# Optimization experiments

Measured on AMD Instinct MI355X. Metric: run time of the kernel, lower is better.

Reference implementation:

```python
import jax, jax.numpy as jnp
import numpy as np

HEADS = 8
DIM_HEAD = 32
TOP_K = 256
KMEANS_ITERS = 10
EPS_LN = 1e-6
EPS_L2 = 1e-12


def chan_layer_norm(x, gamma, beta):
    # x: (b, c, L); normalize across channel dim (biased variance)
    mean = jnp.mean(x, axis=1, keepdims=True)
    var = jnp.var(x, axis=1, keepdims=True)
    return gamma * (x - mean) / (jnp.sqrt(var) + EPS_LN) + beta


def l2norm_ch(t):
    # F.normalize(t, dim=1): L2-normalize over channel axis of (B, c, L)
    n = jnp.linalg.norm(t, axis=1, keepdims=True)
    return t / jnp.maximum(n, EPS_L2)


def conv1x1(x, w):
    # x: (b, c_in, L), w: (c_out, c_in)  -> (b, c_out, L)
    return jnp.einsum('oc,bcl->bol', w, x)


def _dist2(x, c):
    # squared L2 distances, x: (N, d), c: (k, d) -> (N, k)
    return (jnp.sum(x * x, -1, keepdims=True)
            - 2.0 * x @ c.T
            + jnp.sum(c * c, -1)[None, :])


def kmeans_fit(x, k, iters):
    # Lloyd's algorithm, deterministic init = first k points
    c0 = x[:k]

    def step(c, _):
        assign = jnp.argmin(_dist2(x, c), axis=-1)           # (N,)
        sums = jax.ops.segment_sum(x, assign, num_segments=k)
        cnts = jax.ops.segment_sum(jnp.ones((x.shape[0],), x.dtype), assign,
                                   num_segments=k)
        new_c = jnp.where(cnts[:, None] > 0,
                          sums / jnp.maximum(cnts, 1.0)[:, None], c)
        return new_c, None

    c, _ = jax.lax.scan(step, c0, None, length=iters)
    return c


def select_best_ind(q, k, v, top_k):
    # q: (B, Lq, d), k/v: (B, Lk, d); B = b*heads
    B, Lk, d = k.shape
    q_flat = q.reshape(-1, d)
    centroids = kmeans_fit(q_flat, top_k, KMEANS_ITERS)       # (top_k, d)
    k_flat = k.reshape(-1, d)
    k_cluster = jnp.argmin(_dist2(k_flat, centroids), axis=-1).reshape(B, Lk)
    k_centers = centroids[k_cluster]                          # (B, Lk, d)
    k_dist = jnp.sum(jnp.abs(k_centers - k), axis=-1)         # (B, Lk)
    _, best_k = jax.lax.top_k(k_dist, top_k)                  # largest dists
    idx = best_k[:, :, None]
    k_sel = jnp.take_along_axis(k, idx, axis=1)
    v_sel = jnp.take_along_axis(v, idx, axis=1)
    return k_sel, v_sel


def reference(query_source, context, w_q, w_kv, w_out,
              ln_ctx_gamma, ln_ctx_beta, ln_q_gamma, ln_q_beta,
              ln_out_gamma, ln_out_beta, gamma_scale):
    b, c, L_query = query_source.shape
    ctx = chan_layer_norm(context, ln_ctx_gamma, ln_ctx_beta)
    qs = chan_layer_norm(query_source, ln_q_gamma, ln_q_beta)

    kv = conv1x1(ctx, w_kv)                                   # (b, 2*inner, Lc)
    k, v = jnp.split(kv, 2, axis=1)
    q = conv1x1(qs, w_q)                                      # (b, inner, Lq)

    def fold(t):  # b (h c) L -> (b h) c L
        B, hc, L = t.shape
        return t.reshape(B, HEADS, DIM_HEAD, L).reshape(B * HEADS, DIM_HEAD, L)

    q, k, v = fold(q), fold(k), fold(v)
    q, k = l2norm_ch(q), l2norm_ch(k)
    # b d L -> b L d
    q = jnp.swapaxes(q, 1, 2)
    k = jnp.swapaxes(k, 1, 2)
    v = jnp.swapaxes(v, 1, 2)

    k, v = select_best_ind(q, k, v, TOP_K)

    sim = jnp.einsum('bid,bjd->bij', q, k)                    # (b*h, Lq, top_k)
    attn = jax.nn.softmax(sim, axis=-1)
    out = jnp.einsum('bij,bjd->bid', attn, v)                 # (b*h, Lq, dh)

    out = out.reshape(b, HEADS, L_query, DIM_HEAD)
    out = jnp.transpose(out, (0, 1, 3, 2)).reshape(b, HEADS * DIM_HEAD, L_query)
    out = conv1x1(out, w_out)
    out = chan_layer_norm(out, ln_out_gamma, ln_out_beta)
    return gamma_scale[0] * out + query_source


def setup_inputs() -> dict:
    key = jax.random.key(0)
    ks = jax.random.split(key, 8)
    dim, inner = 256, HEADS * DIM_HEAD
    b, Lq, Lc = 2, 4096, 4096
    inp = {
        'query_source': jax.random.normal(ks[0], (b, dim, Lq), jnp.float32),
        'context': jax.random.normal(ks[1], (b, dim, Lc), jnp.float32),
        'w_q': jax.random.normal(ks[2], (inner, dim), jnp.float32) * 0.05,
        'w_kv': jax.random.normal(ks[3], (2 * inner, dim), jnp.float32) * 0.05,
        'w_out': jax.random.normal(ks[4], (dim, inner), jnp.float32) * 0.05,
        'ln_ctx_gamma': jnp.ones((1, dim, 1), jnp.float32),
        'ln_ctx_beta': jnp.zeros((1, dim, 1), jnp.float32),
        'ln_q_gamma': jnp.ones((1, dim, 1), jnp.float32),
        'ln_q_beta': jnp.zeros((1, dim, 1), jnp.float32),
        'ln_out_gamma': jnp.ones((1, dim, 1), jnp.float32),
        'ln_out_beta': jnp.zeros((1, dim, 1), jnp.float32),
        'gamma_scale': jax.random.normal(ks[5], (1,), jnp.float32),
    }
    return inp
```

## Files before the change

kernel.cpp:

```cpp
#include <hip/hip_runtime.h>
#include <math.h>

#define CDIM 256
#define LSEQ 4096
#define NBH 16
#define NPTS 65536
#define KC 256

__device__ __forceinline__ float fadd(float a, float b){ return __fadd_rn(a,b); }
__device__ __forceinline__ float fmul(float a, float b){ return __fmul_rn(a,b); }
__device__ __forceinline__ float fsub(float a, float b){ return __fsub_rn(a,b); }

__device__ __forceinline__ float sum32_np(const float* e){
    float l[16];
    #pragma unroll
    for (int j = 0; j < 16; j++) l[j] = fadd(e[j], e[j + 16]);
    float t3[8];
    #pragma unroll
    for (int j = 0; j < 8; j++) t3[j] = fadd(l[j], l[j + 8]);
    float t6[4];
    #pragma unroll
    for (int j = 0; j < 4; j++) t6[j] = fadd(t3[j], t3[j + 4]);
    return fadd(fadd(t6[0], t6[2]), fadd(t6[1], t6[3]));
}

__global__ __launch_bounds__(64) void ln2_np(
        const float* __restrict__ x0, const float* __restrict__ g0,
        const float* __restrict__ bt0, float* __restrict__ y0,
        const float* __restrict__ x1, const float* __restrict__ g1,
        const float* __restrict__ bt1, float* __restrict__ y1) {
    int gid = blockIdx.x * 64 + threadIdx.x;
    int which = gid >> 13;
    int r = gid & 8191;
    int b = r >> 12, l = r & 4095;
    const float* x  = which ? x1 : x0;
    const float* g  = which ? g1 : g0;
    const float* bt = which ? bt1 : bt0;
    float* y        = which ? y1 : y0;
    const float* xb = x + (size_t)b * CDIM * LSEQ + l;
    float s = 0.f;
    #pragma unroll 8
    for (int c = 0; c < 256; c++) s = fadd(s, xb[(size_t)c * LSEQ]);
    float mean = __fdiv_rn(s, 256.f);
    float s2 = 0.f;
    #pragma unroll 8
    for (int c = 0; c < 256; c++) {
        float d = fsub(xb[(size_t)c * LSEQ], mean);
        s2 = fadd(s2, fmul(d, d));
    }
    float var = __fdiv_rn(s2, 256.f);
    float den = fadd(__fsqrt_rn(var), 1e-6f);
    float* yb = y + (size_t)b * CDIM * LSEQ + l;
    #pragma unroll 4
    for (int c = 0; c < 256; c++) {
        float d = fsub(xb[(size_t)c * LSEQ], mean);
        yb[(size_t)c * LSEQ] = fadd(__fdiv_rn(fmul(g[c], d), den), bt[c]);
    }
}

__global__ __launch_bounds__(256) void conv_all16(
        const float* __restrict__ Wkv, const float* __restrict__ Xkv,
        float* __restrict__ Ykv,
        const float* __restrict__ Wq, const float* __restrict__ Xq,
        float* __restrict__ Yq) {
    __shared__ float ws[16 * 256];
    int tid = threadIdx.x;
    int l0 = blockIdx.x * 512 + tid * 2;
    bool qpath = blockIdx.y >= 32;
    int yb = qpath ? (blockIdx.y - 32) : blockIdx.y;
    int o0 = yb * 16;
    int b = blockIdx.z;
    const float* W = qpath ? Wq : Wkv;
    const float* X = qpath ? Xq : Xkv;
    {
        const float4* wb4 = (const float4*)(W + (size_t)o0 * CDIM);
        float4* ws4s = (float4*)ws;
        for (int i = tid; i < 16 * 64; i += 256) ws4s[i] = wb4[i];
    }
    __syncthreads();
    const float* xb = X + (size_t)b * CDIM * LSEQ;
    float acc[16][2];
    #pragma unroll
    for (int oo = 0; oo < 16; oo++) { acc[oo][0] = 0.f; acc[oo][1] = 0.f; }
    const float4* ws4 = (const float4*)ws;
    bool sop = qpath || (blockIdx.y < 16);
    if (sop) {
        for (int c = 0; c < 256; c += 4) {
            float2 x0q = *(const float2*)(xb + (size_t)(c + 0) * LSEQ + l0);
            float2 x1q = *(const float2*)(xb + (size_t)(c + 1) * LSEQ + l0);
            float2 x2q = *(const float2*)(xb + (size_t)(c + 2) * LSEQ + l0);
            float2 x3q = *(const float2*)(xb + (size_t)(c + 3) * LSEQ + l0);
            #pragma unroll
            for (int oo = 0; oo < 16; oo++) {
                float4 w = ws4[(oo * 256 + c) >> 2];
                acc[oo][0] = fadd(acc[oo][0], fmul(w.x, x0q.x));
                acc[oo][0] = fadd(acc[oo][0], fmul(w.y, x1q.x));
                acc[oo][0] = fadd(acc[oo][0], fmul(w.z, x2q.x));
                acc[oo][0] = fadd(acc[oo][0], fmul(w.w, x3q.x));
                acc[oo][1] = fadd(acc[oo][1], fmul(w.x, x0q.y));
                acc[oo][1] = fadd(acc[oo][1], fmul(w.y, x1q.y));
                acc[oo][1] = fadd(acc[oo][1], fmul(w.z, x2q.y));
                acc[oo][1] = fadd(acc[oo][1], fmul(w.w, x3q.y));
            }
        }
    } else {
        for (int c = 0; c < 256; c += 4) {
            float2 x0q = *(const float2*)(xb + (size_t)(c + 0) * LSEQ + l0);
            float2 x1q = *(const float2*)(xb + (size_t)(c + 1) * LSEQ + l0);
            float2 x2q = *(const float2*)(xb + (size_t)(c + 2) * LSEQ + l0);
            float2 x3q = *(const float2*)(xb + (size_t)(c + 3) * LSEQ + l0);
            #pragma unroll
            for (int oo = 0; oo < 16; oo++) {
                float4 w = ws4[(oo * 256 + c) >> 2];
                acc[oo][0] = __builtin_fmaf(w.x, x0q.x, acc[oo][0]);
                acc[oo][0] = __builtin_fmaf(w.y, x1q.x, acc[oo][0]);
                acc[oo][0] = __builtin_fmaf(w.z, x2q.x, acc[oo][0]);
                acc[oo][0] = __builtin_fmaf(w.w, x3q.x, acc[oo][0]);
                acc[oo][1] = __builtin_fmaf(w.x, x0q.y, acc[oo][1]);
                acc[oo][1] = __builtin_fmaf(w.y, x1q.y, acc[oo][1]);
                acc[oo][1] = __builtin_fmaf(w.z, x2q.y, acc[oo][1]);
                acc[oo][1] = __builtin_fmaf(w.w, x3q.y, acc[oo][1]);
            }
        }
    }
    float* Y = qpath ? Yq : Ykv;
    int rows = qpath ? 256 : 512;
    #pragma unroll
    for (int oo = 0; oo < 16; oo++)
        *(float2*)(Y + ((size_t)b * rows + o0 + oo) * LSEQ + l0) =
            make_float2(acc[oo][0], acc[oo][1]);
}

template<bool EXACT>
__global__ __launch_bounds__(256) void conv_q8(const float* __restrict__ W,
        const float* __restrict__ X, float* __restrict__ Y) {
    __shared__ float ws[8 * 256];
    int tid = threadIdx.x;
    int l0 = blockIdx.x * 1024 + tid * 4;
    int o0 = blockIdx.y * 8;
    int b = blockIdx.z;
    {
        const float4* wb4 = (const float4*)(W + (size_t)o0 * CDIM);
        float4* ws4s = (float4*)ws;
        for (int i = tid; i < 8 * 64; i += 256) ws4s[i] = wb4[i];
    }
    __syncthreads();
    const float* xb = X + (size_t)b * CDIM * LSEQ;
    float acc[8][4];
    #pragma unroll
    for (int oo = 0; oo < 8; oo++)
        #pragma unroll
        for (int i = 0; i < 4; i++) acc[oo][i] = 0.f;
    const float4* ws4 = (const float4*)ws;
    for (int c = 0; c < 256; c += 4) {
        float4 x0q = *(const float4*)(xb + (size_t)(c + 0) * LSEQ + l0);
        float4 x1q = *(const float4*)(xb + (size_t)(c + 1) * LSEQ + l0);
        float4 x2q = *(const float4*)(xb + (size_t)(c + 2) * LSEQ + l0);
        float4 x3q = *(const float4*)(xb + (size_t)(c + 3) * LSEQ + l0);
        #pragma unroll
        for (int oo = 0; oo < 8; oo++) {
            float4 w = ws4[(oo * 256 + c) >> 2];
            if (EXACT) {
                acc[oo][0] = fadd(acc[oo][0], fmul(w.x, x0q.x));
                acc[oo][0] = fadd(acc[oo][0], fmul(w.y, x1q.x));
                acc[oo][0] = fadd(acc[oo][0], fmul(w.z, x2q.x));
                acc[oo][0] = fadd(acc[oo][0], fmul(w.w, x3q.x));
                acc[oo][1] = fadd(acc[oo][1], fmul(w.x, x0q.y));
                acc[oo][1] = fadd(acc[oo][1], fmul(w.y, x1q.y));
                acc[oo][1] = fadd(acc[oo][1], fmul(w.z, x2q.y));
                acc[oo][1] = fadd(acc[oo][1], fmul(w.w, x3q.y));
                acc[oo][2] = fadd(acc[oo][2], fmul(w.x, x0q.z));
                acc[oo][2] = fadd(acc[oo][2], fmul(w.y, x1q.z));
                acc[oo][2] = fadd(acc[oo][2], fmul(w.z, x2q.z));
                acc[oo][2] = fadd(acc[oo][2], fmul(w.w, x3q.z));
                acc[oo][3] = fadd(acc[oo][3], fmul(w.x, x0q.w));
                acc[oo][3] = fadd(acc[oo][3], fmul(w.y, x1q.w));
                acc[oo][3] = fadd(acc[oo][3], fmul(w.z, x2q.w));
                acc[oo][3] = fadd(acc[oo][3], fmul(w.w, x3q.w));
            } else {
                acc[oo][0] = __builtin_fmaf(w.x, x0q.x, acc[oo][0]);
                acc[oo][0] = __builtin_fmaf(w.y, x1q.x, acc[oo][0]);
                acc[oo][0] = __builtin_fmaf(w.z, x2q.x, acc[oo][0]);
                acc[oo][0] = __builtin_fmaf(w.w, x3q.x, acc[oo][0]);
                acc[oo][1] = __builtin_fmaf(w.x, x0q.y, acc[oo][1]);
                acc[oo][1] = __builtin_fmaf(w.y, x1q.y, acc[oo][1]);
                acc[oo][1] = __builtin_fmaf(w.z, x2q.y, acc[oo][1]);
                acc[oo][1] = __builtin_fmaf(w.w, x3q.y, acc[oo][1]);
                acc[oo][2] = __builtin_fmaf(w.x, x0q.z, acc[oo][2]);
                acc[oo][2] = __builtin_fmaf(w.y, x1q.z, acc[oo][2]);
                acc[oo][2] = __builtin_fmaf(w.z, x2q.z, acc[oo][2]);
                acc[oo][2] = __builtin_fmaf(w.w, x3q.z, acc[oo][2]);
                acc[oo][3] = __builtin_fmaf(w.x, x0q.w, acc[oo][3]);
                acc[oo][3] = __builtin_fmaf(w.y, x1q.w, acc[oo][3]);
                acc[oo][3] = __builtin_fmaf(w.z, x2q.w, acc[oo][3]);
                acc[oo][3] = __builtin_fmaf(w.w, x3q.w, acc[oo][3]);
            }
        }
    }
    #pragma unroll
    for (int oo = 0; oo < 8; oo++)
        *(float4*)(Y + ((size_t)b * 256 + o0 + oo) * LSEQ + l0) =
            make_float4(acc[oo][0], acc[oo][1], acc[oo][2], acc[oo][3]);
}

__device__ __forceinline__ void fold_body(const float* __restrict__ src,
        int srcRows, int row0, int donorm, float* __restrict__ dst,
        float* __restrict__ xxout, float* __restrict__ centout,
        float* __restrict__ ccout, int p) {
    int bh = p >> 12, l = p & 4095;
    int b = bh >> 3, h = bh & 7;
    const float* sp = src + ((size_t)b * srcRows + row0 + h * 32) * LSEQ + l;
    float x[32];
    #pragma unroll
    for (int t = 0; t < 32; t++) x[t] = sp[(size_t)t * LSEQ];
    float4* dp4 = (float4*)(dst + (size_t)p * 32);
    if (donorm) {
        float ss = 0.f;
        #pragma unroll
        for (int t = 0; t < 32; t++) ss = fadd(ss, fmul(x[t], x[t]));
        float n = __fsqrt_rn(ss);
        float den = fmaxf(n, 1e-12f);
        #pragma unroll
        for (int t = 0; t < 32; t++) x[t] = __fdiv_rn(x[t], den);
    }
    #pragma unroll
    for (int t = 0; t < 8; t++)
        dp4[t] = make_float4(x[4*t], x[4*t+1], x[4*t+2], x[4*t+3]);
    if (xxout) {
        float e[32];
        #pragma unroll
        for (int t = 0; t < 32; t++) e[t] = fmul(x[t], x[t]);
        float xv = sum32_np(e);
        xxout[p] = xv;
        if (centout && p < KC) {
            float4* cp4 = (float4*)(centout + (size_t)p * 32);
            #pragma unroll
            for (int t = 0; t < 8; t++)
                cp4[t] = make_float4(x[4*t], x[4*t+1], x[4*t+2], x[4*t+3]);
            ccout[p] = xv;
        }
    }
}

__global__ __launch_bounds__(256) void fold3_np(const float* __restrict__ kvbuf,
        const float* __restrict__ qbuf, float* __restrict__ k_t,
        float* __restrict__ v_t, float* __restrict__ q_t,
        float* __restrict__ xx, float* __restrict__ cent, float* __restrict__ cc) {
    int blk = blockIdx.x, tid = threadIdx.x;
    if (blk < 256) {
        fold_body(kvbuf, 512, 0, 1, k_t, nullptr, nullptr, nullptr, blk * 256 + tid);
    } else if (blk < 512) {
        fold_body(kvbuf, 512, 256, 0, v_t, nullptr, nullptr, nullptr, (blk - 256) * 256 + tid);
    } else {
        fold_body(qbuf, 256, 0, 1, q_t, xx, cent, cc, (blk - 512) * 256 + tid);
    }
}

__global__ __launch_bounds__(256) void assign4p(const float* __restrict__ pts,
        const float* __restrict__ xx, const float* __restrict__ cent,
        const float* __restrict__ cc, int* __restrict__ asn, int* __restrict__ hist) {
    __shared__ float sc[8192];
    __shared__ float scc[256];
    __shared__ int bins[256];
    int tid = threadIdx.x, c = blockIdx.x;
    {
        const float4* c4 = (const float4*)cent;
        float4* s4 = (float4*)sc;
        for (int i = tid; i < 2048; i += 256) s4[i] = c4[i];
    }
    scc[tid] = cc[tid];
    bins[tid] = 0;
    __syncthreads();
    int pg = tid >> 2, quarter = tid & 3;
    int pb = c * 256 + pg * 4;
    float x[4][32];
    float xp[4];
    #pragma unroll
    for (int i = 0; i < 4; i++) {
        const float4* pp = (const float4*)(pts + (size_t)(pb + i) * 32);
        #pragma unroll
        for (int t = 0; t < 8; t++) {
            float4 f = pp[t];
            x[i][4*t] = f.x; x[i][4*t+1] = f.y; x[i][4*t+2] = f.z; x[i][4*t+3] = f.w;
        }
        xp[i] = xx[pb + i];
    }
    float bd[4] = {3.4e38f, 3.4e38f, 3.4e38f, 3.4e38f};
    int bj[4] = {0, 0, 0, 0};
    int jbase = quarter * 64;
    for (int jj = 0; jj < 64; jj++) {
        int j = jbase + jj;
        const float4* cj = (const float4*)(sc + j * 32);
        float w[32];
        #pragma unroll
        for (int t = 0; t < 8; t++) {
            float4 f = cj[t];
            w[4*t] = f.x; w[4*t+1] = f.y; w[4*t+2] = f.z; w[4*t+3] = f.w;
        }
        float sj = scc[j];
        #pragma unroll
        for (int i = 0; i < 4; i++) {
            float g = 0.f;
            #pragma unroll
            for (int t = 0; t < 32; t++) g = __builtin_fmaf(x[i][t], w[t], g);
            float d = fadd(fsub(xp[i], fmul(2.f, g)), sj);
            if (d < bd[i]) { bd[i] = d; bj[i] = j; }
        }
    }
    #pragma unroll
    for (int i = 0; i < 4; i++) {
        float ob; int oj;
        ob = __shfl_xor(bd[i], 1); oj = __shfl_xor(bj[i], 1);
        if (ob < bd[i]) { bd[i] = ob; bj[i] = oj; }
        ob = __shfl_xor(bd[i], 2); oj = __shfl_xor(bj[i], 2);
        if (ob < bd[i]) { bd[i] = ob; bj[i] = oj; }
    }
    if (quarter == 0) {
        #pragma unroll
        for (int i = 0; i < 4; i++) {
            asn[pb + i] = bj[i];
            atomicAdd(&bins[bj[i]], 1);
        }
    }
    __syncthreads();
    hist[c * 256 + tid] = bins[tid];
}

__global__ __launch_bounds__(256) void scan_chunks(const int* __restrict__ hist,
        int* __restrict__ chunkbase, int* __restrict__ totals) {
    __shared__ int a[256];
    int j = blockIdx.x, c = threadIdx.x;
    a[c] = hist[(size_t)c * 256 + j];
    __syncthreads();
    for (int d = 1; d < 256; d <<= 1) {
        int v = a[c];
        int u = (c >= d) ? a[c - d] : 0;
        __syncthreads();
        a[c] = v + u;
        __syncthreads();
    }
    chunkbase[(size_t)c * 256 + j] = (c == 0) ? 0 : a[c - 1];
    if (c == 255) totals[j] = a[255];
}

__global__ __launch_bounds__(256) void scatter_v5(const int* __restrict__ asn,
        const int* __restrict__ chunkbase, const int* __restrict__ totals,
        int* __restrict__ perm) {
    __shared__ int cb[256];
    __shared__ int al[256];
    int c = blockIdx.x, tid = threadIdx.x;
    cb[tid] = totals[tid];
    al[tid] = asn[c * 256 + tid];
    __syncthreads();
    for (int d = 1; d < 256; d <<= 1) {
        int v = cb[tid];
        int u = (tid >= d) ? cb[tid - d] : 0;
        __syncthreads();
        cb[tid] = v + u;
        __syncthreads();
    }
    int my = al[tid];
    int base = (my == 0) ? 0 : cb[my - 1];
    int r = 0;
    for (int i = 0; i < tid; i++) r += (al[i] == my) ? 1 : 0;
    perm[base + chunkbase[(size_t)c * 256 + my] + r] = c * 256 + tid;
}

#define STILE 128
__global__ __launch_bounds__(256) void sumk_v4(const float* __restrict__ pts,
        const int* __restrict__ perm, const int* __restrict__ totals,
        float* __restrict__ cent, float* __restrict__ cc) {
    __shared__ int cb[256];
    __shared__ float buf[2][STILE][32];
    int j = blockIdx.x, tid = threadIdx.x;
    cb[tid] = totals[tid];
    __syncthreads();
    for (int d = 1; d < 256; d <<= 1) {
        int v = cb[tid];
        int u = (tid >= d) ? cb[tid - d] : 0;
        __syncthreads();
        cb[tid] = v + u;
        __syncthreads();
    }
    int base = (j == 0) ? 0 : cb[j - 1];
    int n = totals[j];
    int t = tid & 31, r0 = tid >> 5;
    for (int r = r0; r < STILE; r += 8) {
        if (r < n) buf[0][r][t] = pts[(size_t)perm[base + r] * 32 + t];
    }
    __syncthreads();
    float s = 0.f;
    int b = 0;
    for (int i0 = 0; i0 < n; i0 += STILE, b ^= 1) {
        int nx = i0 + STILE;
        if (nx < n) {
            for (int r = r0; r < STILE; r += 8) {
                int g = nx + r;
                if (g < n) buf[b ^ 1][r][t] = pts[(size_t)perm[base + g] * 32 + t];
            }
        }
        if (tid < 32) {
            int m = n - i0; if (m > STILE) m = STILE;
            int i = 0;
            for (; i + 4 <= m; i += 4) {
                s = fadd(s, buf[b][i][tid]);
                s = fadd(s, buf[b][i + 1][tid]);
                s = fadd(s, buf[b][i + 2][tid]);
                s = fadd(s, buf[b][i + 3][tid]);
            }
            for (; i < m; i++) s = fadd(s, buf[b][i][tid]);
        }
        __syncthreads();
    }
    if (tid < 32) {
        float v;
        if (n > 0) {
            v = __fdiv_rn(s, (float)n);
            cent[(size_t)j * 32 + tid] = v;
        } else {
            v = cent[(size_t)j * 32 + tid];
        }
        float e = fmul(v, v);
        e = fadd(e, __shfl_xor(e, 16));
        e = fadd(e, __shfl_xor(e, 8));
        e = fadd(e, __shfl_xor(e, 4));
        e = fadd(e, __shfl_xor(e, 2));
        e = fadd(e, __shfl_xor(e, 1));
        if (tid == 0) cc[j] = e;
    }
}

__global__ __launch_bounds__(256) void kdist4p(const float* __restrict__ pts,
        const float* __restrict__ cent, const float* __restrict__ cc,
        float* __restrict__ kd) {
    __shared__ float sc[8192];
    __shared__ float scc[256];
    int tid = threadIdx.x, c = blockIdx.x;
    {
        const float4* c4 = (const float4*)cent;
        float4* s4 = (float4*)sc;
        for (int i = tid; i < 2048; i += 256) s4[i] = c4[i];
    }
    scc[tid] = cc[tid];
    __syncthreads();
    int pg = tid >> 2, quarter = tid & 3;
    int pb = c * 256 + pg * 4;
    float x[4][32];
    float xp[4];
    #pragma unroll
    for (int i = 0; i < 4; i++) {
        const float4* pp = (const float4*)(pts + (size_t)(pb + i) * 32);
        #pragma unroll
        for (int t = 0; t < 8; t++) {
            float4 f = pp[t];
            x[i][4*t] = f.x; x[i][4*t+1] = f.y; x[i][4*t+2] = f.z; x[i][4*t+3] = f.w;
        }
        float e[32];
        #pragma unroll
        for (int t = 0; t < 32; t++) e[t] = fmul(x[i][t], x[i][t]);
        xp[i] = sum32_np(e);
    }
    float bd[4] = {3.4e38f, 3.4e38f, 3.4e38f, 3.4e38f};
    int bj[4] = {0, 0, 0, 0};
    int jbase = quarter * 64;
    for (int jj = 0; jj < 64; jj++) {
        int j = jbase + jj;
        const float4* cj = (const float4*)(sc + j * 32);
        float w[32];
        #pragma unroll
        for (int t = 0; t < 8; t++) {
            float4 f = cj[t];
            w[4*t] = f.x; w[4*t+1] = f.y; w[4*t+2] = f.z; w[4*t+3] = f.w;
        }
        float sj = scc[j];
        #pragma unroll
        for (int i = 0; i < 4; i++) {
            float g = 0.f;
            #pragma unroll
            for (int t = 0; t < 32; t++) g = __builtin_fmaf(x[i][t], w[t], g);
            float d = fadd(fsub(xp[i], fmul(2.f, g)), sj);
            if (d < bd[i]) { bd[i] = d; bj[i] = j; }
        }
    }
    #pragma unroll
    for (int i = 0; i < 4; i++) {
        float ob; int oj;
        ob = __shfl_xor(bd[i], 1); oj = __shfl_xor(bj[i], 1);
        if (ob < bd[i]) { bd[i] = ob; bj[i] = oj; }
        ob = __shfl_xor(bd[i], 2); oj = __shfl_xor(bj[i], 2);
        if (ob < bd[i]) { bd[i] = ob; bj[i] = oj; }
    }
    if (quarter == 0) {
        #pragma unroll
        for (int i = 0; i < 4; i++) {
            const float* cb = &sc[bj[i] * 32];
            float e[32];
            #pragma unroll
            for (int t = 0; t < 32; t++) e[t] = fabsf(fsub(cb[t], x[i][t]));
            kd[pb + i] = sum32_np(e);
        }
    }
}

__global__ __launch_bounds__(256) void topk_v3(const float* __restrict__ kd,
        const float* __restrict__ k_t, const float* __restrict__ v_t,
        float* __restrict__ ksel, float* __restrict__ vsel) {
    __shared__ int wsum[4];
    __shared__ int sc1[256];
    __shared__ int out_src[256];
    int bh = blockIdx.x, tid = threadIdx.x;
    int wave = tid >> 6, lane = tid & 63;
    unsigned uv[16];
    {
        const unsigned* kdu = (const unsigned*)(kd + (size_t)bh * 4096);
        #pragma unroll
        for (int q = 0; q < 16; q++) uv[q] = kdu[tid * 16 + q];
    }
    unsigned T = 0u;
    for (int bit = 31; bit >= 0; bit--) {
        unsigned cand = T | (1u << bit);
        int c = 0;
        #pragma unroll
        for (int q = 0; q < 16; q++) c += (uv[q] >= cand) ? 1 : 0;
        c += __shfl_xor(c, 32); c += __shfl_xor(c, 16); c += __shfl_xor(c, 8);
        c += __shfl_xor(c, 4);  c += __shfl_xor(c, 2);  c += __shfl_xor(c, 1);
        if (lane == 0) wsum[wave] = c;
        __syncthreads();
        int tot = wsum[0] + wsum[1] + wsum[2] + wsum[3];
        __syncthreads();
        if (tot >= 256) T = cand;
    }
    int r;
    {
        int c = 0;
        #pragma unroll
        for (int q = 0; q < 16; q++) c += (uv[q] > T) ? 1 : 0;
        c += __shfl_xor(c, 32); c += __shfl_xor(c, 16); c += __shfl_xor(c, 8);
        c += __shfl_xor(c, 4);  c += __shfl_xor(c, 2);  c += __shfl_xor(c, 1);
        if (lane == 0) wsum[wave] = c;
        __syncthreads();
        r = 256 - (wsum[0] + wsum[1] + wsum[2] + wsum[3]);
        __syncthreads();
    }
    int ec = 0;
    #pragma unroll
    for (int q = 0; q < 16; q++) ec += (uv[q] == T) ? 1 : 0;
    sc1[tid] = ec;
    __syncthreads();
    for (int d = 1; d < 256; d <<= 1) {
        int t0 = sc1[tid];
        int u0 = (tid >= d) ? sc1[tid - d] : 0;
        __syncthreads();
        sc1[tid] = t0 + u0;
        __syncthreads();
    }
    int erank = (tid == 0) ? 0 : sc1[tid - 1];
    __syncthreads();
    bool incl[16];
    int ic = 0;
    #pragma unroll
    for (int q = 0; q < 16; q++) {
        unsigned u = uv[q];
        bool inc;
        if (u > T) inc = true;
        else if (u == T) { inc = (erank < r); erank++; }
        else inc = false;
        incl[q] = inc;
        ic += inc ? 1 : 0;
    }
    sc1[tid] = ic;
    __syncthreads();
    for (int d = 1; d < 256; d <<= 1) {
        int t0 = sc1[tid];
        int u0 = (tid >= d) ? sc1[tid - d] : 0;
        __syncthreads();
        sc1[tid] = t0 + u0;
        __syncthreads();
    }
    int pos = (tid == 0) ? 0 : sc1[tid - 1];
    int base_i = tid * 16;
    #pragma unroll
    for (int q = 0; q < 16; q++) {
        if (incl[q]) out_src[pos++] = base_i + q;
    }
    __syncthreads();
    for (int e = tid; e < 256 * 32; e += 256) {
        int jj = e >> 5, t = e & 31;
        int src = out_src[jj];
        ksel[(size_t)bh * 8192 + e] = k_t[((size_t)bh * 4096 + src) * 32 + t];
        vsel[(size_t)bh * 8192 + e] = v_t[((size_t)bh * 4096 + src) * 32 + t];
    }
}

#define HP4 2052
__global__ __launch_bounds__(256, 2) void attn_v4(const float* __restrict__ q_t,
        const float* __restrict__ ksel, const float* __restrict__ vsel,
        float* __restrict__ out) {
    __shared__ float sk[4 * HP4];
    __shared__ float sv[4 * HP4];
    int bh = blockIdx.y, tid = threadIdx.x;
    {
        const float4* gk = (const float4*)(ksel + (size_t)bh * 8192);
        const float4* gv = (const float4*)(vsel + (size_t)bh * 8192);
        for (int i = tid; i < 2048; i += 256) {
            int s = i >> 9, idx = i & 511;
            ((float4*)(sk + s * HP4))[idx] = gk[i];
            ((float4*)(sv + s * HP4))[idx] = gv[i];
        }
    }
    __syncthreads();
    int grp = tid >> 3;
    int dh = tid & 1;
    int slice = (tid >> 1) & 3;
    int p0 = bh * 4096 + blockIdx.x * 128 + grp * 4;
    float q[4][16];
    #pragma unroll
    for (int i = 0; i < 4; i++) {
        const float4* qp = (const float4*)(q_t + (size_t)(p0 + i) * 32 + dh * 16);
        #pragma unroll
        for (int t = 0; t < 4; t++) {
            float4 f = qp[t];
            q[i][4*t] = f.x; q[i][4*t+1] = f.y; q[i][4*t+2] = f.z; q[i][4*t+3] = f.w;
        }
    }
    float o[4][16];
    #pragma unroll
    for (int i = 0; i < 4; i++)
        #pragma unroll
        for (int t = 0; t < 16; t++) o[i][t] = 0.f;
    float ls[4] = {0.f, 0.f, 0.f, 0.f};
    const float* kb = sk + slice * HP4 + dh * 16;
    const float* vb = sv + slice * HP4 + dh * 16;
    for (int j = 0; j < 64; j++) {
        float kf[16];
        #pragma unroll
        for (int t = 0; t < 4; t++) {
            float4 f = *(const float4*)(kb + j * 32 + t * 4);
            kf[4*t] = f.x; kf[4*t+1] = f.y; kf[4*t+2] = f.z; kf[4*t+3] = f.w;
        }
        float ps[4];
        #pragma unroll
        for (int i = 0; i < 4; i++) {
            float a = 0.f, b2 = 0.f, c2 = 0.f, d2 = 0.f;
            #pragma unroll
            for (int t = 0; t < 4; t++) {
                a  += q[i][4*t]   * kf[4*t];
                b2 += q[i][4*t+1] * kf[4*t+1];
                c2 += q[i][4*t+2] * kf[4*t+2];
                d2 += q[i][4*t+3] * kf[4*t+3];
            }
            ps[i] = (a + b2) + (c2 + d2);
        }
        #pragma unroll
        for (int i = 0; i < 4; i++) ps[i] += __shfl_xor(ps[i], 1);
        float w[4];
        #pragma unroll
        for (int i = 0; i < 4; i++) {
            w[i] = __expf(ps[i] - 1.0f);
            ls[i] += w[i];
        }
        float vf[16];
        #pragma unroll
        for (int t = 0; t < 4; t++) {
            float4 f = *(const float4*)(vb + j * 32 + t * 4);
            vf[4*t] = f.x; vf[4*t+1] = f.y; vf[4*t+2] = f.z; vf[4*t+3] = f.w;
        }
        #pragma unroll
        for (int i = 0; i < 4; i++)
            #pragma unroll
            for (int t = 0; t < 16; t++) o[i][t] += w[i] * vf[t];
    }
    #pragma unroll
    for (int i = 0; i < 4; i++) {
        #pragma unroll
        for (int t = 0; t < 16; t++) {
            o[i][t] += __shfl_xor(o[i][t], 2);
            o[i][t] += __shfl_xor(o[i][t], 4);
        }
        ls[i] += __shfl_xor(ls[i], 2);
        ls[i] += __shfl_xor(ls[i], 4);
    }
    if (slice == 0) {
        #pragma unroll
        for (int i = 0; i < 4; i++) {
            float inv = 1.f / ls[i];
            float4* op = (float4*)(out + (size_t)(p0 + i) * 32 + dh * 16);
            #pragma unroll
            for (int t = 0; t < 4; t++)
                op[t] = make_float4(o[i][4*t]*inv, o[i][4*t+1]*inv,
                                    o[i][4*t+2]*inv, o[i][4*t+3]*inv);
        }
    }
}

__global__ __launch_bounds__(256) void unfold_kernel(const float* __restrict__ att,
        float* __restrict__ Fo) {
    __shared__ float tbuf[32][65];
    int bh = blockIdx.y, l0 = blockIdx.x * 64;
    int b = bh >> 3, h = bh & 7;
    int tid = threadIdx.x;
    #pragma unroll
    for (int r = 0; r < 8; r++) {
        int e = r * 256 + tid;
        int l = e >> 5, d = e & 31;
        tbuf[d][l] = att[((size_t)bh * 4096 + l0 + l) * 32 + d];
    }
    __syncthreads();
    #pragma unroll
    for (int r = 0; r < 8; r++) {
        int e = r * 256 + tid;
        int d = e >> 6, l = e & 63;
        Fo[((size_t)b * 256 + h * 32 + d) * LSEQ + l0 + l] = tbuf[d][l];
    }
}

__global__ __launch_bounds__(64) void lnres_np(const float* __restrict__ x,
        const float* __restrict__ g, const float* __restrict__ bt,
        const float* __restrict__ gs, const float* __restrict__ qsrc,
        float* __restrict__ y) {
    int gid = blockIdx.x * 64 + threadIdx.x;
    int b = gid >> 12, l = gid & 4095;
    const float* xb = x + (size_t)b * CDIM * LSEQ + l;
    float s = 0.f;
    #pragma unroll 8
    for (int c = 0; c < 256; c++) s = fadd(s, xb[(size_t)c * LSEQ]);
    float mean = __fdiv_rn(s, 256.f);
    float s2 = 0.f;
    #pragma unroll 8
    for (int c = 0; c < 256; c++) {
        float d = fsub(xb[(size_t)c * LSEQ], mean);
        s2 = fadd(s2, fmul(d, d));
    }
    float var = __fdiv_rn(s2, 256.f);
    float den = fadd(__fsqrt_rn(var), 1e-6f);
    float scale = gs[0];
    const float* qb = qsrc + (size_t)b * CDIM * LSEQ + l;
    float* yb = y + (size_t)b * CDIM * LSEQ + l;
    #pragma unroll 4
    for (int c = 0; c < 256; c++) {
        float d = fsub(xb[(size_t)c * LSEQ], mean);
        float r = fadd(__fdiv_rn(fmul(g[c], d), den), bt[c]);
        yb[(size_t)c * LSEQ] = fadd(fmul(scale, r), qb[(size_t)c * LSEQ]);
    }
}

extern "C" void kernel_launch(void* const* d_in, const int* in_sizes, int n_in,
                              void* d_out, int out_size, void* d_ws, size_t ws_size,
                              hipStream_t stream) {
    const float* qsrc   = (const float*)d_in[0];
    const float* ctx    = (const float*)d_in[1];
    const float* w_q    = (const float*)d_in[2];
    const float* w_kv   = (const float*)d_in[3];
    const float* w_out  = (const float*)d_in[4];
    const float* g_ctx  = (const float*)d_in[5];
    const float* b_ctx  = (const float*)d_in[6];
    const float* g_q    = (const float*)d_in[7];
    const float* b_q    = (const float*)d_in[8];
    const float* g_out  = (const float*)d_in[9];
    const float* b_out  = (const float*)d_in[10];
    const float* gs     = (const float*)d_in[11];

    char* base = (char*)d_ws;
    const size_t MB = 1024 * 1024;
    float* yln   = (float*)base;
    float* att   = (float*)base;
    float* kvbuf = (float*)(base + 8 * MB);
    float* y32   = (float*)(base + 8 * MB);
    float* qbuf  = (float*)(base + 24 * MB);
    float* Fo    = (float*)(base + 24 * MB);
    float* q_t   = (float*)(base + 32 * MB);
    float* k_t   = (float*)(base + 40 * MB);
    float* v_t   = (float*)(base + 48 * MB);
    char* SM = base + 56 * MB;
    float* xx_q      = (float*)(SM + 0);
    float* cent      = (float*)(SM + 512 * 1024);
    float* cc        = (float*)(SM + 576 * 1024);
    int*   totals    = (int*)  (SM + 640 * 1024);
    int*   asn       = (int*)  (SM + 704 * 1024);
    int*   hist      = (int*)  (SM + 960 * 1024);
    int*   chunkbase = (int*)  (SM + 1472 * 1024);
    int*   perm      = (int*)  (SM + 1984 * 1024);
    float* kd        = (float*)(SM + 2240 * 1024);
    float* ksel      = (float*)(SM + 2496 * 1024);
    float* vsel      = (float*)(SM + 3008 * 1024);
    float* yln_q     = (float*)(base + 60 * MB);

    ln2_np<<<256, 64, 0, stream>>>(ctx, g_ctx, b_ctx, yln,
                                   qsrc, g_q, b_q, yln_q);
    conv_all16<<<dim3(8, 48, 2), 256, 0, stream>>>(w_kv, yln, kvbuf,
                                                   w_q, yln_q, qbuf);
    fold3_np<<<768, 256, 0, stream>>>(kvbuf, qbuf, k_t, v_t, q_t, xx_q, cent, cc);

    for (int it = 0; it < 10; it++) {
        assign4p<<<256, 256, 0, stream>>>(q_t, xx_q, cent, cc, asn, hist);
        scan_chunks<<<256, 256, 0, stream>>>(hist, chunkbase, totals);
        scatter_v5<<<256, 256, 0, stream>>>(asn, chunkbase, totals, perm);
        sumk_v4<<<256, 256, 0, stream>>>(q_t, perm, totals, cent, cc);
    }

    kdist4p<<<256, 256, 0, stream>>>(k_t, cent, cc, kd);
    topk_v3<<<16, 256, 0, stream>>>(kd, k_t, v_t, ksel, vsel);
    attn_v4<<<dim3(32, 16), 256, 0, stream>>>(q_t, ksel, vsel, att);
    unfold_kernel<<<dim3(64, 16), 256, 0, stream>>>(att, Fo);
    conv_q8<false><<<dim3(4, 32, 2), 256, 0, stream>>>(w_out, Fo, y32);
    lnres_np<<<128, 64, 0, stream>>>(y32, g_out, b_out, gs, qsrc, (float*)d_out);
}
```

Measured before the change: 875.0 us.

## Split k-means assignment over centroid halves and read conv weights directly from global

The k-means assignment kernel now runs twice as many blocks, each scanning half of the centroids. It writes per-half best distances and indices, and a new merge kernel picks the winner and builds the histogram. The aim is more parallelism and occupancy on the 256-CU device, at the cost of an extra launch and extra global traffic per iteration. Separately, the conv kernel drops its shared-memory weight staging and reads weights straight from global memory, relying on caches to serve the reuse and removing a barrier.

```diff
diff --git a/kernel.cpp b/kernel.cpp
--- a/kernel.cpp
+++ b/kernel.cpp
@@ -63,26 +63,18 @@
         float* __restrict__ Ykv,
         const float* __restrict__ Wq, const float* __restrict__ Xq,
         float* __restrict__ Yq) {
-    __shared__ float ws[16 * 256];
     int tid = threadIdx.x;
     int l0 = blockIdx.x * 512 + tid * 2;
     bool qpath = blockIdx.y >= 32;
     int yb = qpath ? (blockIdx.y - 32) : blockIdx.y;
     int o0 = yb * 16;
     int b = blockIdx.z;
-    const float* W = qpath ? Wq : Wkv;
+    const float4* w4 = (const float4*)((qpath ? Wq : Wkv) + (size_t)o0 * CDIM);
     const float* X = qpath ? Xq : Xkv;
-    {
-        const float4* wb4 = (const float4*)(W + (size_t)o0 * CDIM);
-        float4* ws4s = (float4*)ws;
-        for (int i = tid; i < 16 * 64; i += 256) ws4s[i] = wb4[i];
-    }
-    __syncthreads();
     const float* xb = X + (size_t)b * CDIM * LSEQ;
     float acc[16][2];
     #pragma unroll
     for (int oo = 0; oo < 16; oo++) { acc[oo][0] = 0.f; acc[oo][1] = 0.f; }
-    const float4* ws4 = (const float4*)ws;
     bool sop = qpath || (blockIdx.y < 16);
     if (sop) {
         for (int c = 0; c < 256; c += 4) {
@@ -92,7 +84,7 @@
             float2 x3q = *(const float2*)(xb + (size_t)(c + 3) * LSEQ + l0);
             #pragma unroll
             for (int oo = 0; oo < 16; oo++) {
-                float4 w = ws4[(oo * 256 + c) >> 2];
+                float4 w = w4[(oo * 256 + c) >> 2];
                 acc[oo][0] = fadd(acc[oo][0], fmul(w.x, x0q.x));
                 acc[oo][0] = fadd(acc[oo][0], fmul(w.y, x1q.x));
                 acc[oo][0] = fadd(acc[oo][0], fmul(w.z, x2q.x));
@@ -111,7 +103,7 @@
             float2 x3q = *(const float2*)(xb + (size_t)(c + 3) * LSEQ + l0);
             #pragma unroll
             for (int oo = 0; oo < 16; oo++) {
-                float4 w = ws4[(oo * 256 + c) >> 2];
+                float4 w = w4[(oo * 256 + c) >> 2];
                 acc[oo][0] = __builtin_fmaf(w.x, x0q.x, acc[oo][0]);
                 acc[oo][0] = __builtin_fmaf(w.y, x1q.x, acc[oo][0]);
                 acc[oo][0] = __builtin_fmaf(w.z, x2q.x, acc[oo][0]);
@@ -256,20 +248,19 @@
     }
 }
 
-__global__ __launch_bounds__(256) void assign4p(const float* __restrict__ pts,
+__global__ __launch_bounds__(256) void assign_h(const float* __restrict__ pts,
         const float* __restrict__ xx, const float* __restrict__ cent,
-        const float* __restrict__ cc, int* __restrict__ asn, int* __restrict__ hist) {
-    __shared__ float sc[8192];
-    __shared__ float scc[256];
-    __shared__ int bins[256];
-    int tid = threadIdx.x, c = blockIdx.x;
+        const float* __restrict__ cc, float* __restrict__ bdg, int* __restrict__ bjg) {
+    __shared__ float sc[4096];
+    __shared__ float scc[128];
+    int tid = threadIdx.x;
+    int c = blockIdx.x >> 1, h = blockIdx.x & 1;
     {
-        const float4* c4 = (const float4*)cent;
+        const float4* c4 = (const float4*)(cent + (size_t)h * 128 * 32);
         float4* s4 = (float4*)sc;
-        for (int i = tid; i < 2048; i += 256) s4[i] = c4[i];
-    }
-    scc[tid] = cc[tid];
-    bins[tid] = 0;
+        for (int i = tid; i < 1024; i += 256) s4[i] = c4[i];
+    }
+    if (tid < 128) scc[tid] = cc[h * 128 + tid];
     __syncthreads();
     int pg = tid >> 2, quarter = tid & 3;
     int pb = c * 256 + pg * 4;
@@ -287,8 +278,8 @@
     }
     float bd[4] = {3.4e38f, 3.4e38f, 3.4e38f, 3.4e38f};
     int bj[4] = {0, 0, 0, 0};
-    int jbase = quarter * 64;
-    for (int jj = 0; jj < 64; jj++) {
+    int jbase = quarter * 32;
+    for (int jj = 0; jj < 32; jj++) {
         int j = jbase + jj;
         const float4* cj = (const float4*)(sc + j * 32);
         float w[32];
@@ -298,13 +289,14 @@
             w[4*t] = f.x; w[4*t+1] = f.y; w[4*t+2] = f.z; w[4*t+3] = f.w;
         }
         float sj = scc[j];
+        int jg = h * 128 + j;
         #pragma unroll
         for (int i = 0; i < 4; i++) {
             float g = 0.f;
             #pragma unroll
             for (int t = 0; t < 32; t++) g = __builtin_fmaf(x[i][t], w[t], g);
             float d = fadd(fsub(xp[i], fmul(2.f, g)), sj);
-            if (d < bd[i]) { bd[i] = d; bj[i] = j; }
+            if (d < bd[i]) { bd[i] = d; bj[i] = jg; }
         }
     }
     #pragma unroll
@@ -318,10 +310,23 @@
     if (quarter == 0) {
         #pragma unroll
         for (int i = 0; i < 4; i++) {
-            asn[pb + i] = bj[i];
-            atomicAdd(&bins[bj[i]], 1);
-        }
-    }
+            bdg[(size_t)h * NPTS + pb + i] = bd[i];
+            bjg[(size_t)h * NPTS + pb + i] = bj[i];
+        }
+    }
+}
+
+__global__ __launch_bounds__(256) void merge_asn(const float* __restrict__ bdg,
+        const int* __restrict__ bjg, int* __restrict__ asn, int* __restrict__ hist) {
+    __shared__ int bins[256];
+    int tid = threadIdx.x, c = blockIdx.x;
+    bins[tid] = 0;
+    __syncthreads();
+    int p = c * 256 + tid;
+    float d0 = bdg[p], d1 = bdg[NPTS + p];
+    int j = (d1 < d0) ? bjg[NPTS + p] : bjg[p];
+    asn[p] = j;
+    atomicAdd(&bins[j], 1);
     __syncthreads();
     hist[c * 256 + tid] = bins[tid];
 }
@@ -766,6 +771,8 @@
     float* att   = (float*)base;
     float* kvbuf = (float*)(base + 8 * MB);
     float* y32   = (float*)(base + 8 * MB);
+    float* bdg   = (float*)(base + 8 * MB);
+    int*   bjg   = (int*)  (base + 9 * MB);
     float* qbuf  = (float*)(base + 24 * MB);
     float* Fo    = (float*)(base + 24 * MB);
     float* q_t   = (float*)(base + 32 * MB);
@@ -792,7 +799,8 @@
     fold3_np<<<768, 256, 0, stream>>>(kvbuf, qbuf, k_t, v_t, q_t, xx_q, cent, cc);
 
     for (int it = 0; it < 10; it++) {
-        assign4p<<<256, 256, 0, stream>>>(q_t, xx_q, cent, cc, asn, hist);
+        assign_h<<<512, 256, 0, stream>>>(q_t, xx_q, cent, cc, bdg, bjg);
+        merge_asn<<<256, 256, 0, stream>>>(bdg, bjg, asn, hist);
         scan_chunks<<<256, 256, 0, stream>>>(hist, chunkbase, totals);
         scatter_v5<<<256, 256, 0, stream>>>(asn, chunkbase, totals, perm);
         sumk_v4<<<256, 256, 0, stream>>>(q_t, perm, totals, cent, cc);
```

After: 880.1 us. Within noise of the previous version (+0.6%).
